# Performance work log

Hardware: AMD Instinct MI355X
Metric: run time of the kernel (lower is better)

The kernel has to match this reference:

```python
import jax, jax.numpy as jnp
import numpy as np

B, S, D = 64, 2048, 512


def setup_inputs() -> dict:
    key = jax.random.key(0)
    k1, k2, k3, k4 = jax.random.split(key, 4)
    decoder_output = jax.random.normal(k1, (B, 1, D), dtype=jnp.float32)
    encoder_output = jax.random.normal(k2, (B, S, D), dtype=jnp.float32)
    # W_a_tanh: Dense(D) applied to concat([dec, enc]) of width 2D
    scale_w = 1.0 / np.sqrt(2 * D)
    W_t = jax.random.normal(k3, (2 * D, D), dtype=jnp.float32) * scale_w
    b_t = jnp.zeros((D,), dtype=jnp.float32)
    # v_a: Dense(1)
    v_a = jax.random.normal(k4, (D, 1), dtype=jnp.float32) * (1.0 / np.sqrt(D))
    b_v = jnp.zeros((1,), dtype=jnp.float32)
    return {
        "decoder_output": decoder_output,
        "encoder_output": encoder_output,
        "W_t": W_t,
        "b_t": b_t,
        "v_a": v_a,
        "b_v": b_v,
    }


def reference(decoder_output, encoder_output, W_t, b_t, v_a, b_v):
    # concat-variant Luong attention
    dec = jnp.broadcast_to(decoder_output, encoder_output.shape)       # [B,S,D]
    concated = jnp.concatenate((dec, encoder_output), axis=-1)          # [B,S,2D]
    hidden = jnp.tanh(jnp.einsum('bse,ed->bsd', concated, W_t) + b_t)   # [B,S,D]
    score = (jnp.einsum('bsd,do->bso', hidden, v_a) + b_v)              # [B,S,1]
    score = jnp.transpose(score, (0, 2, 1))                             # [B,1,S]
    alignment_vector = jax.nn.softmax(score, axis=2)                    # [B,1,S]
    context_vector = jnp.matmul(alignment_vector, encoder_output)       # [B,1,D]
    return (context_vector, alignment_vector)
```

## Files before the change

### kernel.cpp

```cpp
#include <hip/hip_runtime.h>

#define BB 64
#define SS 2048
#define DD 512

typedef __attribute__((ext_vector_type(8))) short bf16x8;
typedef __attribute__((ext_vector_type(4))) float f32x4;

__device__ __forceinline__ unsigned f2bf(float f) {
    unsigned u = __float_as_uint(f);
    u += 0x7FFFu + ((u >> 16) & 1u);
    return u >> 16;
}

__device__ __forceinline__ float fast_tanh(float x) {
    float ax = fabsf(x);
    float e = __expf(-2.0f * ax);
    float t = (1.0f - e) * __builtin_amdgcn_rcpf(1.0f + e);
    return x < 0.0f ? -t : t;
}

__global__ void prep_w(const float* __restrict__ W, short* __restrict__ Bt) {
    __shared__ float tile[64][65];
    int kt = blockIdx.x >> 3;
    int nt = blockIdx.x & 7;
    int t = threadIdx.x;
    int c = t & 63;
    int rbase = (t >> 6) * 16;
    #pragma unroll
    for (int i = 0; i < 16; ++i) {
        int r = rbase + i;
        tile[r][c] = W[(size_t)(512 + kt * 64 + r) * DD + nt * 64 + c];
    }
    __syncthreads();
    #pragma unroll
    for (int i = 0; i < 16; ++i) {
        int r = rbase + i;
        Bt[(size_t)(nt * 64 + r) * DD + kt * 64 + c] = (short)f2bf(tile[c][r]);
    }
}

__global__ void prep_p(const float* __restrict__ dec, const float* __restrict__ W,
                       const float* __restrict__ bt, float* __restrict__ p) {
    int b = blockIdx.x;
    int d = blockIdx.y * 256 + threadIdx.x;
    float acc = bt[d];
    const float* dv = dec + (size_t)b * DD;
    #pragma unroll 8
    for (int e = 0; e < DD; ++e)
        acc += dv[e] * W[(size_t)e * DD + d];
    p[(size_t)b * DD + d] = acc;
}

__device__ __forceinline__ void write_slab(char* AhiB, char* AloB, unsigned off, f32x4 x) {
    unsigned hb0 = f2bf(x.x), hb1 = f2bf(x.y), hb2 = f2bf(x.z), hb3 = f2bf(x.w);
    uint2 hv;
    hv.x = hb0 | (hb1 << 16);
    hv.y = hb2 | (hb3 << 16);
    float r0 = x.x - __uint_as_float(hb0 << 16);
    float r1 = x.y - __uint_as_float(hb1 << 16);
    float r2 = x.z - __uint_as_float(hb2 << 16);
    float r3 = x.w - __uint_as_float(hb3 << 16);
    uint2 lv;
    lv.x = f2bf(r0) | (f2bf(r1) << 16);
    lv.y = f2bf(r2) | (f2bf(r3) << 16);
    *(uint2*)(AhiB + off) = hv;
    *(uint2*)(AloB + off) = lv;
}

__global__ __launch_bounds__(512, 2)
void fused_k(const float* __restrict__ enc, const short* __restrict__ Bt,
             const float* __restrict__ p, const float* __restrict__ va,
             float* __restrict__ score, float* __restrict__ ml,
             float* __restrict__ pctx) {
    __shared__ short Ahi[64 * 512];
    __shared__ short Alo[64 * 512];
    __shared__ float sp[8][64];
    __shared__ float elds[64];
    __shared__ float sp2[4][512];

    const int tid  = threadIdx.x;
    const int wave = tid >> 6;
    const int lane = tid & 63;
    const int lm   = lane & 15;
    const int lq   = lane >> 4;
    const int blk  = blockIdx.x;
    const int b    = blk >> 5;
    const size_t m0 = (size_t)blk * 64;

    char* AhiB = (char*)Ahi;
    char* AloB = (char*)Alo;

    const int srow = tid >> 3;
    const int skc8 = (tid & 7) * 8;
    const unsigned srowB = (unsigned)srow * 1024;
    const unsigned swsr  = (unsigned)(srow & 7) << 4;
    const float* aptr = enc + m0 * DD + (size_t)srow * DD + (tid & 7) * 4;

    const unsigned lq16 = (unsigned)lq * 16;
    const unsigned swlm = (unsigned)(lm & 7) << 4;
    unsigned arow[4];
    #pragma unroll
    for (int mf = 0; mf < 4; ++mf) arow[mf] = (unsigned)(mf * 16 + lm) * 1024;
    const short* Bw = Bt + (size_t)(wave * 64 + lm) * DD + lq * 8;

    f32x4 acc[4][4];
    #pragma unroll
    for (int i = 0; i < 4; ++i)
        #pragma unroll
        for (int j = 0; j < 4; ++j)
            acc[i][j] = (f32x4){0.f, 0.f, 0.f, 0.f};

    f32x4 stg[2];
    stg[0] = *(const f32x4*)(aptr);
    stg[1] = *(const f32x4*)(aptr + 32);
    write_slab(AhiB, AloB, srowB + ((unsigned)skc8 ^ swsr), stg[0]);
    __syncthreads();

    #pragma unroll
    for (int kt = 0; kt < 16; ++kt) {
        if (kt < 14) stg[kt & 1] = *(const f32x4*)(aptr + (kt + 2) * 32);
        const unsigned kx = ((unsigned)(kt * 64) + lq16) ^ swlm;
        bf16x8 af[4];
        #pragma unroll
        for (int mf = 0; mf < 4; ++mf)
            af[mf] = *(const bf16x8*)(AhiB + (arow[mf] + kx));
        #pragma unroll
        for (int nf = 0; nf < 4; ++nf) {
            bf16x8 bfr = *(const bf16x8*)(Bw + nf * 16 * DD + kt * 32);
            #pragma unroll
            for (int mf = 0; mf < 4; ++mf)
                acc[mf][nf] = __builtin_amdgcn_mfma_f32_16x16x32_bf16(af[mf], bfr, acc[mf][nf], 0, 0, 0);
        }
        if (kt < 15) {
            unsigned off = srowB + (((unsigned)((kt + 1) * 64 + skc8)) ^ swsr);
            write_slab(AhiB, AloB, off, stg[(kt + 1) & 1]);
        }
        __syncthreads();
    }

    const float* pb = p + (size_t)b * DD;
    float rowsum[4][4];
    #pragma unroll
    for (int mf = 0; mf < 4; ++mf)
        #pragma unroll
        for (int r = 0; r < 4; ++r) rowsum[mf][r] = 0.f;

    #pragma unroll
    for (int nf = 0; nf < 4; ++nf) {
        int n = wave * 64 + nf * 16 + lm;
        float pv = pb[n];
        float vv = va[n];
        #pragma unroll
        for (int mf = 0; mf < 4; ++mf)
            #pragma unroll
            for (int r = 0; r < 4; ++r)
                rowsum[mf][r] += fast_tanh(pv + acc[mf][nf][r]) * vv;
    }
    #pragma unroll
    for (int mf = 0; mf < 4; ++mf)
        #pragma unroll
        for (int r = 0; r < 4; ++r) {
            float s = rowsum[mf][r];
            s += __shfl_xor(s, 1);
            s += __shfl_xor(s, 2);
            s += __shfl_xor(s, 4);
            s += __shfl_xor(s, 8);
            rowsum[mf][r] = s;
        }
    if (lm == 0) {
        #pragma unroll
        for (int mf = 0; mf < 4; ++mf)
            #pragma unroll
            for (int r = 0; r < 4; ++r)
                sp[wave][mf * 16 + lq * 4 + r] = rowsum[mf][r];
    }
    __syncthreads();

    if (tid < 64) {
        float s = 0.f;
        #pragma unroll
        for (int w = 0; w < 8; ++w) s += sp[w][tid];
        score[m0 + tid] = s;
        float mx = s;
        #pragma unroll
        for (int off = 32; off > 0; off >>= 1) mx = fmaxf(mx, __shfl_xor(mx, off));
        float e = __expf(s - mx);
        float l = e;
        #pragma unroll
        for (int off = 32; off > 0; off >>= 1) l += __shfl_xor(l, off);
        elds[tid] = e;
        if (tid == 0) {
            ml[(size_t)blk * 2]     = mx;
            ml[(size_t)blk * 2 + 1] = l;
        }
    }
    __syncthreads();

    {
        const int q = tid & 127;
        const int g = tid >> 7;
        const unsigned dbyte = (unsigned)q * 8;
        float c0 = 0.f, c1 = 0.f, c2 = 0.f, c3 = 0.f;
        #pragma unroll
        for (int si = 0; si < 16; ++si) {
            int s = g * 16 + si;
            float ev = elds[s];
            unsigned off = (unsigned)s * 1024 + (dbyte ^ ((unsigned)(s & 7) << 4));
            uint2 hv = *(const uint2*)(AhiB + off);
            uint2 lv = *(const uint2*)(AloB + off);
            c0 += ev * (__uint_as_float(hv.x << 16) + __uint_as_float(lv.x << 16));
            c1 += ev * (__uint_as_float(hv.x & 0xffff0000u) + __uint_as_float(lv.x & 0xffff0000u));
            c2 += ev * (__uint_as_float(hv.y << 16) + __uint_as_float(lv.y << 16));
            c3 += ev * (__uint_as_float(hv.y & 0xffff0000u) + __uint_as_float(lv.y & 0xffff0000u));
        }
        *(f32x4*)(&sp2[g][q * 4]) = (f32x4){c0, c1, c2, c3};
    }
    __syncthreads();
    {
        float v = sp2[0][tid] + sp2[1][tid] + sp2[2][tid] + sp2[3][tid];
        pctx[(size_t)blk * 512 + tid] = v;
    }
}

__global__ void combine_k(const float* __restrict__ score, const float* __restrict__ ml,
                          const float* __restrict__ pctx, float* __restrict__ ctx,
                          float* __restrict__ align) {
    __shared__ float sc[32];
    __shared__ float MB, LB;
    const int b = blockIdx.x, tid = threadIdx.x;
    if (tid < 32) sc[tid] = ml[(size_t)(b * 32 + tid) * 2];
    __syncthreads();
    if (tid == 0) {
        float M = sc[0];
        #pragma unroll
        for (int i = 1; i < 32; ++i) M = fmaxf(M, sc[i]);
        float L = 0.f;
        for (int i = 0; i < 32; ++i) {
            float w = __expf(sc[i] - M);
            L += w * ml[(size_t)(b * 32 + i) * 2 + 1];
            sc[i] = w;
        }
        MB = M;
        LB = L;
    }
    __syncthreads();
    const float M = MB, Linv = 1.0f / LB;
    float a0 = 0.f, a1 = 0.f;
    for (int i = 0; i < 32; ++i) {
        float w = sc[i];
        const float* pc = pctx + (size_t)(b * 32 + i) * 512;
        a0 += w * pc[tid];
        a1 += w * pc[tid + 256];
    }
    ctx[(size_t)b * DD + tid]       = a0 * Linv;
    ctx[(size_t)b * DD + tid + 256] = a1 * Linv;
    const float* sr = score + (size_t)b * SS;
    float* al = align + (size_t)b * SS;
    #pragma unroll
    for (int i = 0; i < 8; ++i) {
        int s = i * 256 + tid;
        al[s] = __expf(sr[s] - M) * Linv;
    }
}

extern "C" void kernel_launch(void* const* d_in, const int* in_sizes, int n_in,
                              void* d_out, int out_size, void* d_ws, size_t ws_size,
                              hipStream_t stream) {
    const float* dec = (const float*)d_in[0];
    const float* enc = (const float*)d_in[1];
    const float* W   = (const float*)d_in[2];
    const float* bt  = (const float*)d_in[3];
    const float* va  = (const float*)d_in[4];

    float* out   = (float*)d_out;
    float* ctx   = out;
    float* align = out + BB * DD;

    char*  ws    = (char*)d_ws;
    short* Bt    = (short*)ws;
    float* p     = (float*)(ws + 524288);
    float* score = (float*)(ws + 655360);
    float* ml    = (float*)(ws + 1179648);
    float* pctx  = (float*)(ws + 1196032);

    prep_w<<<64, 256, 0, stream>>>(W, Bt);
    prep_p<<<dim3(BB, 2), 256, 0, stream>>>(dec, W, bt, p);
    fused_k<<<BB * 32, 512, 0, stream>>>(enc, Bt, p, va, score, ml, pctx);
    combine_k<<<BB, 256, 0, stream>>>(score, ml, pctx, ctx, align);
}
```

Measured before the change: 554.8 us.

## Keep encoder tile in registers, drop lo-bf16 slab, use 1024-thread blocks

The fused kernel now launches 1024 threads per block, each holding eight float4 chunks of its encoder row in registers for the whole kernel. It stores only the high bf16 half in LDS, dropping the Alo buffer and halving LDS traffic and footprint. The MFMA work is split 2x8 across waves, with each k-step covering 128 columns. The context partial sum is built from the fp32 register copy using shuffles and an LDS reduction over 16 waves, not by re-reading LDS. This trades more registers per thread and an extra reduction stage for less LDS use, fewer conversions, and possibly more blocks resident per CU.

```diff
diff --git a/kernel.cpp b/kernel.cpp
--- a/kernel.cpp
+++ b/kernel.cpp
@@ -52,113 +52,111 @@
     p[(size_t)b * DD + d] = acc;
 }
 
-__device__ __forceinline__ void write_slab(char* AhiB, char* AloB, unsigned off, f32x4 x) {
-    unsigned hb0 = f2bf(x.x), hb1 = f2bf(x.y), hb2 = f2bf(x.z), hb3 = f2bf(x.w);
-    uint2 hv;
-    hv.x = hb0 | (hb1 << 16);
-    hv.y = hb2 | (hb3 << 16);
-    float r0 = x.x - __uint_as_float(hb0 << 16);
-    float r1 = x.y - __uint_as_float(hb1 << 16);
-    float r2 = x.z - __uint_as_float(hb2 << 16);
-    float r3 = x.w - __uint_as_float(hb3 << 16);
-    uint2 lv;
-    lv.x = f2bf(r0) | (f2bf(r1) << 16);
-    lv.y = f2bf(r2) | (f2bf(r3) << 16);
-    *(uint2*)(AhiB + off) = hv;
-    *(uint2*)(AloB + off) = lv;
-}
-
-__global__ __launch_bounds__(512, 2)
+__global__ __launch_bounds__(1024, 4)
 void fused_k(const float* __restrict__ enc, const short* __restrict__ Bt,
              const float* __restrict__ p, const float* __restrict__ va,
              float* __restrict__ score, float* __restrict__ ml,
              float* __restrict__ pctx) {
-    __shared__ short Ahi[64 * 512];
-    __shared__ short Alo[64 * 512];
-    __shared__ float sp[8][64];
-    __shared__ float elds[64];
-    __shared__ float sp2[4][512];
+    __shared__ char smem[65536 + 2048 + 256];
+    char* AhiB = smem;
+    float (*red)[512] = (float (*)[512])smem;
+    float (*sp)[32]   = (float (*)[32])(smem + 65536);
+    float* elds       = (float*)(smem + 67584);
 
     const int tid  = threadIdx.x;
     const int wave = tid >> 6;
     const int lane = tid & 63;
     const int lm   = lane & 15;
     const int lq   = lane >> 4;
+    const int wm   = wave >> 3;
+    const int wn   = wave & 7;
     const int blk  = blockIdx.x;
     const int b    = blk >> 5;
     const size_t m0 = (size_t)blk * 64;
 
-    char* AhiB = (char*)Ahi;
-    char* AloB = (char*)Alo;
-
-    const int srow = tid >> 3;
-    const int skc8 = (tid & 7) * 8;
-    const unsigned srowB = (unsigned)srow * 1024;
+    const int srow = tid >> 4;
+    const int sc   = tid & 15;
+    const unsigned srowB = (unsigned)srow * 1024u;
     const unsigned swsr  = (unsigned)(srow & 7) << 4;
-    const float* aptr = enc + m0 * DD + (size_t)srow * DD + (tid & 7) * 4;
-
-    const unsigned lq16 = (unsigned)lq * 16;
+    const float* aptr = enc + (m0 + (size_t)srow) * DD + sc * 4;
+
     const unsigned swlm = (unsigned)(lm & 7) << 4;
-    unsigned arow[4];
-    #pragma unroll
-    for (int mf = 0; mf < 4; ++mf) arow[mf] = (unsigned)(mf * 16 + lm) * 1024;
-    const short* Bw = Bt + (size_t)(wave * 64 + lm) * DD + lq * 8;
-
-    f32x4 acc[4][4];
-    #pragma unroll
-    for (int i = 0; i < 4; ++i)
+    const unsigned arow0 = (unsigned)(wm * 32 + lm) * 1024u;
+    const unsigned arow1 = arow0 + 16u * 1024u;
+    const short* Bw = Bt + (size_t)(wn * 64 + lm) * DD + lq * 8;
+
+    f32x4 acc[2][4];
+    #pragma unroll
+    for (int i = 0; i < 2; ++i)
         #pragma unroll
         for (int j = 0; j < 4; ++j)
             acc[i][j] = (f32x4){0.f, 0.f, 0.f, 0.f};
 
-    f32x4 stg[2];
-    stg[0] = *(const f32x4*)(aptr);
-    stg[1] = *(const f32x4*)(aptr + 32);
-    write_slab(AhiB, AloB, srowB + ((unsigned)skc8 ^ swsr), stg[0]);
-    __syncthreads();
-
-    #pragma unroll
-    for (int kt = 0; kt < 16; ++kt) {
-        if (kt < 14) stg[kt & 1] = *(const f32x4*)(aptr + (kt + 2) * 32);
-        const unsigned kx = ((unsigned)(kt * 64) + lq16) ^ swlm;
-        bf16x8 af[4];
-        #pragma unroll
-        for (int mf = 0; mf < 4; ++mf)
-            af[mf] = *(const bf16x8*)(AhiB + (arow[mf] + kx));
+    f32x4 stg[8];
+    #pragma unroll
+    for (int s = 0; s < 4; ++s)
+        stg[s] = *(const f32x4*)(aptr + s * 64);
+    {
+        uint2 hv;
+        hv.x = f2bf(stg[0].x) | (f2bf(stg[0].y) << 16);
+        hv.y = f2bf(stg[0].z) | (f2bf(stg[0].w) << 16);
+        *(uint2*)(AhiB + (srowB + ((sc * 8u) ^ swsr))) = hv;
+    }
+    __syncthreads();
+
+    #pragma unroll
+    for (int kt = 0; kt < 8; ++kt) {
+        if (kt < 4)
+            stg[kt + 4] = *(const f32x4*)(aptr + (kt + 4) * 64);
+
+        const unsigned kb = (unsigned)kt * 128u;
+        bf16x8 af[2][2];
+        af[0][0] = *(const bf16x8*)(AhiB + arow0 + ((kb + 0u  + lq * 16u) ^ swlm));
+        af[0][1] = *(const bf16x8*)(AhiB + arow0 + ((kb + 64u + lq * 16u) ^ swlm));
+        af[1][0] = *(const bf16x8*)(AhiB + arow1 + ((kb + 0u  + lq * 16u) ^ swlm));
+        af[1][1] = *(const bf16x8*)(AhiB + arow1 + ((kb + 64u + lq * 16u) ^ swlm));
+
         #pragma unroll
         for (int nf = 0; nf < 4; ++nf) {
-            bf16x8 bfr = *(const bf16x8*)(Bw + nf * 16 * DD + kt * 32);
-            #pragma unroll
-            for (int mf = 0; mf < 4; ++mf)
-                acc[mf][nf] = __builtin_amdgcn_mfma_f32_16x16x32_bf16(af[mf], bfr, acc[mf][nf], 0, 0, 0);
-        }
-        if (kt < 15) {
-            unsigned off = srowB + (((unsigned)((kt + 1) * 64 + skc8)) ^ swsr);
-            write_slab(AhiB, AloB, off, stg[(kt + 1) & 1]);
+            const short* bp = Bw + nf * 16 * DD + kt * 64;
+            bf16x8 b0 = *(const bf16x8*)(bp);
+            bf16x8 b1 = *(const bf16x8*)(bp + 32);
+            acc[0][nf] = __builtin_amdgcn_mfma_f32_16x16x32_bf16(af[0][0], b0, acc[0][nf], 0, 0, 0);
+            acc[1][nf] = __builtin_amdgcn_mfma_f32_16x16x32_bf16(af[1][0], b0, acc[1][nf], 0, 0, 0);
+            acc[0][nf] = __builtin_amdgcn_mfma_f32_16x16x32_bf16(af[0][1], b1, acc[0][nf], 0, 0, 0);
+            acc[1][nf] = __builtin_amdgcn_mfma_f32_16x16x32_bf16(af[1][1], b1, acc[1][nf], 0, 0, 0);
+        }
+
+        if (kt < 7) {
+            f32x4 x = stg[kt + 1];
+            uint2 hv;
+            hv.x = f2bf(x.x) | (f2bf(x.y) << 16);
+            hv.y = f2bf(x.z) | (f2bf(x.w) << 16);
+            *(uint2*)(AhiB + (srowB + (((unsigned)((kt + 1) * 128) + sc * 8u) ^ swsr))) = hv;
         }
         __syncthreads();
     }
 
     const float* pb = p + (size_t)b * DD;
-    float rowsum[4][4];
-    #pragma unroll
-    for (int mf = 0; mf < 4; ++mf)
+    float rowsum[2][4];
+    #pragma unroll
+    for (int mf = 0; mf < 2; ++mf)
         #pragma unroll
         for (int r = 0; r < 4; ++r) rowsum[mf][r] = 0.f;
 
     #pragma unroll
     for (int nf = 0; nf < 4; ++nf) {
-        int n = wave * 64 + nf * 16 + lm;
+        int n = wn * 64 + nf * 16 + lm;
         float pv = pb[n];
         float vv = va[n];
         #pragma unroll
-        for (int mf = 0; mf < 4; ++mf)
+        for (int mf = 0; mf < 2; ++mf)
             #pragma unroll
             for (int r = 0; r < 4; ++r)
                 rowsum[mf][r] += fast_tanh(pv + acc[mf][nf][r]) * vv;
     }
     #pragma unroll
-    for (int mf = 0; mf < 4; ++mf)
+    for (int mf = 0; mf < 2; ++mf)
         #pragma unroll
         for (int r = 0; r < 4; ++r) {
             float s = rowsum[mf][r];
@@ -170,7 +168,7 @@
         }
     if (lm == 0) {
         #pragma unroll
-        for (int mf = 0; mf < 4; ++mf)
+        for (int mf = 0; mf < 2; ++mf)
             #pragma unroll
             for (int r = 0; r < 4; ++r)
                 sp[wave][mf * 16 + lq * 4 + r] = rowsum[mf][r];
@@ -178,9 +176,11 @@
     __syncthreads();
 
     if (tid < 64) {
+        const int base = (tid >> 5) * 8;
+        const int rl = tid & 31;
         float s = 0.f;
         #pragma unroll
-        for (int w = 0; w < 8; ++w) s += sp[w][tid];
+        for (int w = 0; w < 8; ++w) s += sp[base + w][rl];
         score[m0 + tid] = s;
         float mx = s;
         #pragma unroll
@@ -198,27 +198,26 @@
     __syncthreads();
 
     {
-        const int q = tid & 127;
-        const int g = tid >> 7;
-        const unsigned dbyte = (unsigned)q * 8;
-        float c0 = 0.f, c1 = 0.f, c2 = 0.f, c3 = 0.f;
-        #pragma unroll
-        for (int si = 0; si < 16; ++si) {
-            int s = g * 16 + si;
-            float ev = elds[s];
-            unsigned off = (unsigned)s * 1024 + (dbyte ^ ((unsigned)(s & 7) << 4));
-            uint2 hv = *(const uint2*)(AhiB + off);
-            uint2 lv = *(const uint2*)(AloB + off);
-            c0 += ev * (__uint_as_float(hv.x << 16) + __uint_as_float(lv.x << 16));
-            c1 += ev * (__uint_as_float(hv.x & 0xffff0000u) + __uint_as_float(lv.x & 0xffff0000u));
-            c2 += ev * (__uint_as_float(hv.y << 16) + __uint_as_float(lv.y << 16));
-            c3 += ev * (__uint_as_float(hv.y & 0xffff0000u) + __uint_as_float(lv.y & 0xffff0000u));
-        }
-        *(f32x4*)(&sp2[g][q * 4]) = (f32x4){c0, c1, c2, c3};
-    }
-    __syncthreads();
-    {
-        float v = sp2[0][tid] + sp2[1][tid] + sp2[2][tid] + sp2[3][tid];
+        float ev = elds[srow];
+        #pragma unroll
+        for (int s = 0; s < 8; ++s) {
+            float v0 = ev * stg[s].x;
+            float v1 = ev * stg[s].y;
+            float v2 = ev * stg[s].z;
+            float v3 = ev * stg[s].w;
+            v0 += __shfl_xor(v0, 16); v0 += __shfl_xor(v0, 32);
+            v1 += __shfl_xor(v1, 16); v1 += __shfl_xor(v1, 32);
+            v2 += __shfl_xor(v2, 16); v2 += __shfl_xor(v2, 32);
+            v3 += __shfl_xor(v3, 16); v3 += __shfl_xor(v3, 32);
+            if (lane < 16)
+                *(f32x4*)(&red[wave][s * 64 + sc * 4]) = (f32x4){v0, v1, v2, v3};
+        }
+    }
+    __syncthreads();
+    if (tid < 512) {
+        float v = 0.f;
+        #pragma unroll
+        for (int w = 0; w < 16; ++w) v += red[w][tid];
         pctx[(size_t)blk * 512 + tid] = v;
     }
 }
@@ -286,6 +285,6 @@
 
     prep_w<<<64, 256, 0, stream>>>(W, Bt);
     prep_p<<<dim3(BB, 2), 256, 0, stream>>>(dec, W, bt, p);
-    fused_k<<<BB * 32, 512, 0, stream>>>(enc, Bt, p, va, score, ml, pctx);
+    fused_k<<<BB * 32, 1024, 0, stream>>>(enc, Bt, p, va, score, ml, pctx);
     combine_k<<<BB, 256, 0, stream>>>(score, ml, pctx, ctx, align);
 }
```

Measured after the change: 656.2 us. +18.3%, slower.
